# Performance work log

Hardware: AMD Instinct MI355X
Metric: run time of the kernel (lower is better)

## Reference

```python
import jax
import jax.numpy as jnp
from jax import lax
import numpy as np

E = 4          # num_experts
CIN = 128
COUT = 128
K = 3
STAT = 6
HID = 16       # router hidden width
STRIDE = 1
PAD = 1


def setup_inputs() -> dict:
    key = jax.random.key(0)
    ks = jax.random.split(key, 8)
    B, H, W = 32, 64, 64
    x = jax.random.normal(ks[0], (B, CIN, H, W), dtype=jnp.float32)
    scene_stats = jax.random.normal(ks[1], (B, STAT), dtype=jnp.float32)
    # router: Linear(stat_dim,16) -> ReLU -> Linear(16,E) -> Softmax
    W1 = jax.random.normal(ks[2], (HID, STAT), dtype=jnp.float32) * (1.0 / np.sqrt(STAT))
    b1 = jnp.zeros((HID,), dtype=jnp.float32)
    W2 = jax.random.normal(ks[3], (E, HID), dtype=jnp.float32) * (1.0 / np.sqrt(HID))
    b2 = jnp.zeros((E,), dtype=jnp.float32)
    weight_experts = jax.random.normal(ks[4], (E, COUT, CIN, K, K), dtype=jnp.float32) * 0.02
    bias_experts = jnp.zeros((E, COUT), dtype=jnp.float32)
    return {"x": x, "scene_stats": scene_stats, "W1": W1, "b1": b1,
            "W2": W2, "b2": b2, "weight_experts": weight_experts,
            "bias_experts": bias_experts}


def reference(x, scene_stats, W1, b1, W2, b2, weight_experts, bias_experts):
    B, Cin, H, W = x.shape
    Cout = weight_experts.shape[1]
    # router
    h = jax.nn.relu(scene_stats @ W1.T + b1)                 # [B, HID]
    routing = jax.nn.softmax(h @ W2.T + b2, axis=1)          # [B, E]
    # per-sample dynamic weights / bias
    dyn_w = jnp.einsum('bk,koihw->boihw', routing, weight_experts)  # [B,Cout,Cin,K,K]
    dyn_b = jnp.einsum('bk,ko->bo', routing, bias_experts)          # [B,Cout]
    # grouped conv with groups = B (each sample uses its own filter bank)
    x_r = x.reshape(1, B * Cin, H, W)
    w_r = dyn_w.reshape(B * Cout, Cin, K, K)
    out = lax.conv_general_dilated(
        x_r, w_r,
        window_strides=(STRIDE, STRIDE),
        padding=((PAD, PAD), (PAD, PAD)),
        feature_group_count=B,
        dimension_numbers=('NCHW', 'OIHW', 'NCHW'))
    out = out.reshape(B, Cout, out.shape[2], out.shape[3])
    return out + dyn_b[:, :, None, None]
```

## Files before the change

kernel.cpp:

```cpp
#include <hip/hip_runtime.h>
#include <hip/hip_bf16.h>


typedef short bf16x8 __attribute__((ext_vector_type(8)));
typedef float f32x4  __attribute__((ext_vector_type(4)));

#define VMWAIT(n) asm volatile("s_waitcnt vmcnt(" #n ")" ::: "memory")
#define LGKM0()   asm volatile("s_waitcnt lgkmcnt(0)" ::: "memory")

static __device__ __forceinline__ unsigned short f2bf(float f) {
    unsigned u = __float_as_uint(f);
    u = u + 0x7FFFu + ((u >> 16) & 1u);
    return (unsigned short)(u >> 16);
}

static __device__ __forceinline__ void gl2lds16(const unsigned short* g, unsigned short* l) {
    __builtin_amdgcn_global_load_lds(
        (const __attribute__((address_space(1))) unsigned int*)g,
        (__attribute__((address_space(3))) unsigned int*)l,
        16, 0, 0);
}

__global__ void prep_kernel(const float* __restrict__ stats, const float* __restrict__ W1,
                            const float* __restrict__ b1, const float* __restrict__ W2,
                            const float* __restrict__ b2, const float* __restrict__ wexp,
                            const float* __restrict__ bexp, unsigned short* __restrict__ dynw,
                            float* __restrict__ dynb)
{
    __shared__ float ls[4*1152];
    __shared__ float lr[32*4];
    const int tid = threadIdx.x;
    const int co  = blockIdx.x & 127;
    const int bg  = blockIdx.x >> 7;

    if (tid < 32) {
        float s[6];
#pragma unroll
        for (int i = 0; i < 6; ++i) s[i] = stats[tid*6 + i];
        float h[16];
#pragma unroll
        for (int j = 0; j < 16; ++j) {
            float a = b1[j];
#pragma unroll
            for (int i = 0; i < 6; ++i) a += W1[j*6+i]*s[i];
            h[j] = a > 0.f ? a : 0.f;
        }
        float lg[4];
#pragma unroll
        for (int e = 0; e < 4; ++e) {
            float a = b2[e];
#pragma unroll
            for (int j = 0; j < 16; ++j) a += W2[e*16+j]*h[j];
            lg[e] = a;
        }
        float m = fmaxf(fmaxf(lg[0],lg[1]), fmaxf(lg[2],lg[3]));
        float ex[4], sum = 0.f;
#pragma unroll
        for (int e = 0; e < 4; ++e) { ex[e] = expf(lg[e]-m); sum += ex[e]; }
        float inv = 1.f / sum;
#pragma unroll
        for (int e = 0; e < 4; ++e) lr[tid*4+e] = ex[e]*inv;
    }
    for (int i = tid; i < 4*1152; i += 256) {
        int e = i / 1152, j = i - e*1152;
        ls[i] = wexp[((unsigned long long)(e*128 + co))*1152 + j];
    }
    __syncthreads();

    if (bg == 0 && tid < 32) {
        float sb = 0.f;
#pragma unroll
        for (int e = 0; e < 4; ++e) sb += lr[tid*4+e] * bexp[e*128 + co];
        dynb[tid*128 + co] = sb;
    }

    const int ci  = tid & 127;
    const int tp0 = tid >> 7;
    const int cic = ci >> 5;
    const int g   = (ci >> 3) & 3;
    const int jj  = ci & 7;
    const int mi  = co >> 4;
    const int l15 = co & 15;
    for (int bb = bg*8; bb < bg*8 + 8; ++bb) {
        float r0 = lr[bb*4+0], r1 = lr[bb*4+1], r2 = lr[bb*4+2], r3 = lr[bb*4+3];
#pragma unroll
        for (int pp = 0; pp < 5; ++pp) {
            int tap = 2*pp + tp0;
            if (tap < 9) {
                int j = ci*9 + tap;
                float v = r0*ls[j] + r1*ls[1152+j] + r2*ls[2*1152+j] + r3*ls[3*1152+j];
                dynw[((((unsigned long long)(bb*4 + cic)*9 + tap)*8 + mi)*64 + g*16 + l15)*8 + jj] = f2bf(v);
            }
        }
    }
}

__global__ __launch_bounds__(256, 2) void conv_kernel(
    const float* __restrict__ x,
    const unsigned short* __restrict__ dynw,
    const float* __restrict__ dynb,
    float* __restrict__ out)
{
    __shared__ __align__(16) unsigned short xs[6*66*40];
    __shared__ __align__(16) unsigned short wsm[6][4096];

    const int tid  = threadIdx.x;
    const int wave = tid >> 6;
    const int lane = tid & 63;
    const int l15  = lane & 15;
    const int g    = lane >> 4;
    const int pr   = tid >> 4;
    const int c4   = tid & 15;

    int bidx = ((blockIdx.x & 7) << 6) | (blockIdx.x >> 3);
    const int b  = bidx >> 4;
    const int r0 = (bidx & 15) << 2;

    f32x4 acc[8][4];
#pragma unroll
    for (int mi = 0; mi < 8; ++mi)
#pragma unroll
        for (int ni = 0; ni < 4; ++ni) acc[mi][ni] = (f32x4){0.f,0.f,0.f,0.f};

    const float* xsrcb = x + (unsigned long long)b*(128ull*64*64);
    const unsigned short* wsrcb = dynw + (unsigned long long)b*(4ull*9*4096);

    float4 xvA[2][2];
    float4 xvB[4][2];

#define XISSUE(CIC_, KK, DST)                                                  \
    do {                                                                       \
        int grow_ = r0 + (KK) - 1;                                             \
        int growc_ = grow_ < 0 ? 0 : (grow_ > 63 ? 63 : grow_);                \
        const float* xp_ = xsrcb + (unsigned)(((CIC_)*32 + 2*pr)*4096)         \
                         + growc_*64 + c4*4;                                   \
        DST[0] = *(const float4*)xp_;                                          \
        DST[1] = *(const float4*)(xp_ + 4096);                                 \
    } while (0)

#define XPACK(KK, SRC)                                                         \
    do {                                                                       \
        int grow_ = r0 + (KK) - 1;                                             \
        bool oob_ = (grow_ < 0) || (grow_ > 63);                               \
        float4 va_ = SRC[0], vb_ = SRC[1];                                     \
        unsigned w0_ = oob_ ? 0u : (f2bf(va_.x) | ((unsigned)f2bf(vb_.x) << 16)); \
        unsigned w1_ = oob_ ? 0u : (f2bf(va_.y) | ((unsigned)f2bf(vb_.y) << 16)); \
        unsigned w2_ = oob_ ? 0u : (f2bf(va_.z) | ((unsigned)f2bf(vb_.z) << 16)); \
        unsigned w3_ = oob_ ? 0u : (f2bf(va_.w) | ((unsigned)f2bf(vb_.w) << 16)); \
        char* bp_ = (char*)xs + (KK)*5280 + (4*c4 + 1)*80 + pr*4;              \
        *(unsigned*)(bp_)       = w0_;                                         \
        *(unsigned*)(bp_ + 80)  = w1_;                                         \
        *(unsigned*)(bp_ + 160) = w2_;                                         \
        *(unsigned*)(bp_ + 240) = w3_;                                         \
    } while (0)

    if (tid < 60) {
        int r = tid / 10, rem = tid - r*10;
        int col = (rem < 5) ? 0 : 65;
        int qq  = (rem < 5) ? rem : rem - 5;
        *(uint4*)((char*)xs + r*5280 + col*80 + qq*16) = make_uint4(0,0,0,0);
    }
    XISSUE(0,0,xvA[0]); XISSUE(0,1,xvA[1]);
    XISSUE(0,2,xvB[0]); XISSUE(0,3,xvB[1]); XISSUE(0,4,xvB[2]); XISSUE(0,5,xvB[3]);
#pragma unroll
    for (int t = 0; t < 3; ++t) {
        const unsigned short* wsrc = wsrcb + (unsigned)(t*4096);
        gl2lds16(wsrc + (unsigned)tid*8,       wsm[t] + (unsigned)tid*8);
        gl2lds16(wsrc + (unsigned)(tid+256)*8, wsm[t] + (unsigned)(tid+256)*8);
    }
    VMWAIT(6);
    XPACK(0,xvA[0]); XPACK(1,xvA[1]);
    XPACK(2,xvB[0]); XPACK(3,xvB[1]); XPACK(4,xvB[2]); XPACK(5,xvB[3]);
    VMWAIT(0);
    LGKM0();
    __builtin_amdgcn_s_barrier();
    __builtin_amdgcn_sched_barrier(0);

#pragma unroll
    for (int p = 0; p < 12; ++p) {
        const int cic = p / 3;
        const int q   = p % 3;
        if (p > 0) {
            VMWAIT(0);
            __builtin_amdgcn_s_barrier();
            __builtin_amdgcn_sched_barrier(0);
        }
        if (q == 0 && p > 0) {
            XPACK(2,xvB[0]); XPACK(3,xvB[1]); XPACK(4,xvB[2]); XPACK(5,xvB[3]);
            LGKM0();
            __builtin_amdgcn_s_barrier();
            __builtin_amdgcn_sched_barrier(0);
        }
        if (p < 11) {
#pragma unroll
            for (int t = 0; t < 3; ++t) {
                const int s = 3*p + 3 + t;
                const unsigned short* wsrc = wsrcb + (unsigned)(s*4096);
                unsigned short* wd = wsm[s % 6];
                gl2lds16(wsrc + (unsigned)tid*8,       wd + (unsigned)tid*8);
                gl2lds16(wsrc + (unsigned)(tid+256)*8, wd + (unsigned)(tid+256)*8);
            }
        }
        if (q == 1 && cic < 3) {
            XISSUE(cic+1,0,xvA[0]); XISSUE(cic+1,1,xvA[1]);
            __builtin_amdgcn_sched_barrier(0);
        }
        if (q == 2 && cic < 3) {
            XPACK(0,xvA[0]); XPACK(1,xvA[1]);
            XISSUE(cic+1,2,xvB[0]); XISSUE(cic+1,3,xvB[1]);
            XISSUE(cic+1,4,xvB[2]); XISSUE(cic+1,5,xvB[3]);
            __builtin_amdgcn_sched_barrier(0);
        }
        const int lrow = wave + q;
        __builtin_amdgcn_s_setprio(1);
#pragma unroll
        for (int kx = 0; kx < 3; ++kx) {
            const unsigned short* wb = wsm[(3*p + kx) % 6];
            bf16x8 bfr[4];
#pragma unroll
            for (int ni = 0; ni < 4; ++ni) {
                int lcol = 16*ni + l15 + kx;
                bfr[ni] = *(const bf16x8*)((const char*)xs
                              + lrow*5280 + lcol*80 + g*16);
            }
#pragma unroll
            for (int mi = 0; mi < 8; ++mi) {
                bf16x8 afrag = *(const bf16x8*)(wb + (unsigned)((mi*64 + lane)*8));
#pragma unroll
                for (int ni = 0; ni < 4; ++ni)
                    acc[mi][ni] = __builtin_amdgcn_mfma_f32_16x16x32_bf16(
                                      afrag, bfr[ni], acc[mi][ni], 0, 0, 0);
            }
        }
        __builtin_amdgcn_s_setprio(0);
    }

    const int y = r0 + wave;
#pragma unroll
    for (int mi = 0; mi < 8; ++mi) {
#pragma unroll
        for (int r = 0; r < 4; ++r) {
            int co = 16*mi + g*4 + r;
            float bias = dynb[b*128 + co];
            float* op = out + (((unsigned long long)(b*128 + co))*64 + y)*64;
#pragma unroll
            for (int ni = 0; ni < 4; ++ni)
                op[16*ni + l15] = acc[mi][ni][r] + bias;
        }
    }
#undef XPACK
#undef XISSUE
}

extern "C" void kernel_launch(void* const* d_in, const int* in_sizes, int n_in,
                              void* d_out, int out_size, void* d_ws, size_t ws_size,
                              hipStream_t stream)
{
    const float* x     = (const float*)d_in[0];
    const float* stats = (const float*)d_in[1];
    const float* W1    = (const float*)d_in[2];
    const float* b1    = (const float*)d_in[3];
    const float* W2    = (const float*)d_in[4];
    const float* b2    = (const float*)d_in[5];
    const float* wexp  = (const float*)d_in[6];
    const float* bexp  = (const float*)d_in[7];
    float* out = (float*)d_out;

    char* ws = (char*)d_ws;
    float* dynb           = (float*)(ws + 512);
    unsigned short* dynw  = (unsigned short*)(ws + 32768);

    prep_kernel<<<512, 256, 0, stream>>>(stats, W1, b1, W2, b2, wexp, bexp, dynw, dynb);
    conv_kernel<<<512, 256, 0, stream>>>(x, dynw, dynb, out);
}
```

Baseline: 58.90 us.

## Restructure x staging to scalar loads with 16-byte LDS stores, halve prep grid

The input staging changes from float4 row loads packed as 4-byte LDS stores to per-thread scalar loads across 8 channels, packed into a single 16-byte LDS store per row. This cuts LDS write instructions and possible bank conflicts, but uses more global load instructions with less vector width. The MFMA loop now loads two A fragments at a time to give more independent MFMAs per load. The prep kernel covers 16 batches per block with half as many blocks, which means fewer redundant loads of the expert weights.

Result: slower. 63.13 us (+7.2%).

```diff
diff --git a/kernel.cpp b/kernel.cpp
--- a/kernel.cpp
+++ b/kernel.cpp
@@ -81,7 +81,7 @@
     const int jj  = ci & 7;
     const int mi  = co >> 4;
     const int l15 = co & 15;
-    for (int bb = bg*8; bb < bg*8 + 8; ++bb) {
+    for (int bb = bg*16; bb < bg*16 + 16; ++bb) {
         float r0 = lr[bb*4+0], r1 = lr[bb*4+1], r2 = lr[bb*4+2], r3 = lr[bb*4+3];
 #pragma unroll
         for (int pp = 0; pp < 5; ++pp) {
@@ -109,8 +109,8 @@
     const int lane = tid & 63;
     const int l15  = lane & 15;
     const int g    = lane >> 4;
-    const int pr   = tid >> 4;
-    const int c4   = tid & 15;
+    const int sa   = tid >> 6;
+    const int scol = tid & 63;
 
     int bidx = ((blockIdx.x & 7) << 6) | (blockIdx.x >> 3);
     const int b  = bidx >> 4;
@@ -125,33 +125,31 @@
     const float* xsrcb = x + (unsigned long long)b*(128ull*64*64);
     const unsigned short* wsrcb = dynw + (unsigned long long)b*(4ull*9*4096);
 
-    float4 xvA[2][2];
-    float4 xvB[4][2];
+    float xA[2][8];
+    float xB[4][8];
 
 #define XISSUE(CIC_, KK, DST)                                                  \
     do {                                                                       \
         int grow_ = r0 + (KK) - 1;                                             \
         int growc_ = grow_ < 0 ? 0 : (grow_ > 63 ? 63 : grow_);                \
-        const float* xp_ = xsrcb + (unsigned)(((CIC_)*32 + 2*pr)*4096)         \
-                         + growc_*64 + c4*4;                                   \
-        DST[0] = *(const float4*)xp_;                                          \
-        DST[1] = *(const float4*)(xp_ + 4096);                                 \
+        const float* xp_ = xsrcb + (unsigned)(((CIC_)*32 + sa*8)*4096)         \
+                         + growc_*64 + scol;                                   \
+        DST[0] = xp_[0];       DST[1] = xp_[4096];                             \
+        DST[2] = xp_[2*4096];  DST[3] = xp_[3*4096];                           \
+        DST[4] = xp_[4*4096];  DST[5] = xp_[5*4096];                           \
+        DST[6] = xp_[6*4096];  DST[7] = xp_[7*4096];                           \
     } while (0)
 
 #define XPACK(KK, SRC)                                                         \
     do {                                                                       \
         int grow_ = r0 + (KK) - 1;                                             \
         bool oob_ = (grow_ < 0) || (grow_ > 63);                               \
-        float4 va_ = SRC[0], vb_ = SRC[1];                                     \
-        unsigned w0_ = oob_ ? 0u : (f2bf(va_.x) | ((unsigned)f2bf(vb_.x) << 16)); \
-        unsigned w1_ = oob_ ? 0u : (f2bf(va_.y) | ((unsigned)f2bf(vb_.y) << 16)); \
-        unsigned w2_ = oob_ ? 0u : (f2bf(va_.z) | ((unsigned)f2bf(vb_.z) << 16)); \
-        unsigned w3_ = oob_ ? 0u : (f2bf(va_.w) | ((unsigned)f2bf(vb_.w) << 16)); \
-        char* bp_ = (char*)xs + (KK)*5280 + (4*c4 + 1)*80 + pr*4;              \
-        *(unsigned*)(bp_)       = w0_;                                         \
-        *(unsigned*)(bp_ + 80)  = w1_;                                         \
-        *(unsigned*)(bp_ + 160) = w2_;                                         \
-        *(unsigned*)(bp_ + 240) = w3_;                                         \
+        unsigned w0_ = oob_ ? 0u : (f2bf(SRC[0]) | ((unsigned)f2bf(SRC[1]) << 16)); \
+        unsigned w1_ = oob_ ? 0u : (f2bf(SRC[2]) | ((unsigned)f2bf(SRC[3]) << 16)); \
+        unsigned w2_ = oob_ ? 0u : (f2bf(SRC[4]) | ((unsigned)f2bf(SRC[5]) << 16)); \
+        unsigned w3_ = oob_ ? 0u : (f2bf(SRC[6]) | ((unsigned)f2bf(SRC[7]) << 16)); \
+        *(uint4*)((char*)xs + (KK)*5280 + (scol + 1)*80 + sa*16)               \
+            = make_uint4(w0_, w1_, w2_, w3_);                                  \
     } while (0)
 
     if (tid < 60) {
@@ -160,8 +158,8 @@
         int qq  = (rem < 5) ? rem : rem - 5;
         *(uint4*)((char*)xs + r*5280 + col*80 + qq*16) = make_uint4(0,0,0,0);
     }
-    XISSUE(0,0,xvA[0]); XISSUE(0,1,xvA[1]);
-    XISSUE(0,2,xvB[0]); XISSUE(0,3,xvB[1]); XISSUE(0,4,xvB[2]); XISSUE(0,5,xvB[3]);
+    XISSUE(0,0,xA[0]); XISSUE(0,1,xA[1]);
+    XISSUE(0,2,xB[0]); XISSUE(0,3,xB[1]); XISSUE(0,4,xB[2]); XISSUE(0,5,xB[3]);
 #pragma unroll
     for (int t = 0; t < 3; ++t) {
         const unsigned short* wsrc = wsrcb + (unsigned)(t*4096);
@@ -169,8 +167,8 @@
         gl2lds16(wsrc + (unsigned)(tid+256)*8, wsm[t] + (unsigned)(tid+256)*8);
     }
     VMWAIT(6);
-    XPACK(0,xvA[0]); XPACK(1,xvA[1]);
-    XPACK(2,xvB[0]); XPACK(3,xvB[1]); XPACK(4,xvB[2]); XPACK(5,xvB[3]);
+    XPACK(0,xA[0]); XPACK(1,xA[1]);
+    XPACK(2,xB[0]); XPACK(3,xB[1]); XPACK(4,xB[2]); XPACK(5,xB[3]);
     VMWAIT(0);
     LGKM0();
     __builtin_amdgcn_s_barrier();
@@ -186,7 +184,7 @@
             __builtin_amdgcn_sched_barrier(0);
         }
         if (q == 0 && p > 0) {
-            XPACK(2,xvB[0]); XPACK(3,xvB[1]); XPACK(4,xvB[2]); XPACK(5,xvB[3]);
+            XPACK(2,xB[0]); XPACK(3,xB[1]); XPACK(4,xB[2]); XPACK(5,xB[3]);
             LGKM0();
             __builtin_amdgcn_s_barrier();
             __builtin_amdgcn_sched_barrier(0);
@@ -202,13 +200,13 @@
             }
         }
         if (q == 1 && cic < 3) {
-            XISSUE(cic+1,0,xvA[0]); XISSUE(cic+1,1,xvA[1]);
+            XISSUE(cic+1,0,xA[0]); XISSUE(cic+1,1,xA[1]);
             __builtin_amdgcn_sched_barrier(0);
         }
         if (q == 2 && cic < 3) {
-            XPACK(0,xvA[0]); XPACK(1,xvA[1]);
-            XISSUE(cic+1,2,xvB[0]); XISSUE(cic+1,3,xvB[1]);
-            XISSUE(cic+1,4,xvB[2]); XISSUE(cic+1,5,xvB[3]);
+            XPACK(0,xA[0]); XPACK(1,xA[1]);
+            XISSUE(cic+1,2,xB[0]); XISSUE(cic+1,3,xB[1]);
+            XISSUE(cic+1,4,xB[2]); XISSUE(cic+1,5,xB[3]);
             __builtin_amdgcn_sched_barrier(0);
         }
         const int lrow = wave + q;
@@ -224,12 +222,17 @@
                               + lrow*5280 + lcol*80 + g*16);
             }
 #pragma unroll
-            for (int mi = 0; mi < 8; ++mi) {
-                bf16x8 afrag = *(const bf16x8*)(wb + (unsigned)((mi*64 + lane)*8));
+            for (int mh = 0; mh < 4; ++mh) {
+                bf16x8 af0 = *(const bf16x8*)(wb + (unsigned)(((2*mh)*64 + lane)*8));
+                bf16x8 af1 = *(const bf16x8*)(wb + (unsigned)(((2*mh+1)*64 + lane)*8));
 #pragma unroll
                 for (int ni = 0; ni < 4; ++ni)
-                    acc[mi][ni] = __builtin_amdgcn_mfma_f32_16x16x32_bf16(
-                                      afrag, bfr[ni], acc[mi][ni], 0, 0, 0);
+                    acc[2*mh][ni] = __builtin_amdgcn_mfma_f32_16x16x32_bf16(
+                                        af0, bfr[ni], acc[2*mh][ni], 0, 0, 0);
+#pragma unroll
+                for (int ni = 0; ni < 4; ++ni)
+                    acc[2*mh+1][ni] = __builtin_amdgcn_mfma_f32_16x16x32_bf16(
+                                        af1, bfr[ni], acc[2*mh+1][ni], 0, 0, 0);
             }
         }
         __builtin_amdgcn_s_setprio(0);
@@ -270,6 +273,6 @@
     float* dynb           = (float*)(ws + 512);
     unsigned short* dynw  = (unsigned short*)(ws + 32768);
 
-    prep_kernel<<<512, 256, 0, stream>>>(stats, W1, b1, W2, b2, wexp, bexp, dynw, dynb);
+    prep_kernel<<<256, 256, 0, stream>>>(stats, W1, b1, W2, b2, wexp, bexp, dynw, dynb);
     conv_kernel<<<512, 256, 0, stream>>>(x, dynw, dynb, out);
 }
```
